# Optimization experiments

Hardware: AMD Instinct MI355X
Metric: run time of the kernel (lower is better)

## Reference

```python
import jax, jax.numpy as jnp
import numpy as np


def setup_inputs() -> dict:
    key = jax.random.key(0)
    k1, k2, k3 = jax.random.split(key, 3)
    B, N, D = 4, 4096, 256
    val = jax.random.normal(k1, (B, N, D), dtype=jnp.float32)
    state = jax.random.normal(k2, (B, N), dtype=jnp.float32)
    # val projection weight, scaled for unit-variance outputs
    Wv = jax.random.normal(k3, (D, D), dtype=jnp.float32) / np.sqrt(D)
    return {"val": val, "state": state, "Wv": Wv}


def reference(val, state, Wv):
    # pairwise_fn: dot-product scores over all node pairs -> [B, N, N]
    scores = jnp.einsum("bnd,bmd->bnm", val, val)
    # edge_compress_fn: softsign (non-softmax elementwise nonlinearity)
    edges = scores / (1.0 + jnp.abs(scores))
    # state_proj_fn = identity, val_proj_fn = linear
    projected_state = state                                  # [B, N]
    projected_val = jnp.einsum("bmd,de->bme", val, Wv)       # [B, N, D]
    # dual aggregation reusing the same edge matrix
    delta_state = jnp.einsum("bnm,bm->bn", edges, projected_state)
    delta_val = jnp.einsum("bnm,bmd->bnd", edges, projected_val)
    return (delta_state, delta_val)
```

## Files before the change

kernel.cpp:

```cpp
#include <hip/hip_runtime.h>

typedef unsigned short u16;
typedef unsigned char u8;
typedef unsigned int u32;
typedef __bf16 bf16x8 __attribute__((ext_vector_type(8)));
typedef float  f32x16 __attribute__((ext_vector_type(16)));
typedef int    i32x4  __attribute__((ext_vector_type(4)));
typedef int    i32x16 __attribute__((ext_vector_type(16)));

#define NB 4
#define NN 4096
#define ND 256

#define QPV (127.0f / 4.5f)
#define DPV (4.5f / 16129.0f)
#define QST (127.0f / 4.6f)
#define DST (4.6f / 16129.0f)
#define MAGIC 12582912.0f

__device__ __forceinline__ u16 f2bf(float x) { return __builtin_bit_cast(u16, (__bf16)x); }
__device__ __forceinline__ u32 fbits(float x) { return __builtin_bit_cast(u32, x); }

__device__ __forceinline__ u32 packlow4(float a, float b, float c, float d) {
    u32 p = __builtin_amdgcn_perm(fbits(b), fbits(a), 0x00000400u);
    u32 q = __builtin_amdgcn_perm(fbits(d), fbits(c), 0x00000400u);
    return __builtin_amdgcn_perm(q, p, 0x05040100u);
}


__global__ __launch_bounds__(256) void k_prep(const float* __restrict__ val,
                                              const float* __restrict__ state,
                                              const float* __restrict__ Wv,
                                              u16* __restrict__ kq, u8* __restrict__ kq8,
                                              float* __restrict__ srow,
                                              u8* __restrict__ vp8, u16* __restrict__ wv) {
    int tid = threadIdx.x;
    int bid = blockIdx.x;
    if (bid < 512) {
        __shared__ float t[32 * 257];
        __shared__ float rmax[32];
        const float* src = val + (size_t)bid * 32 * 256;
        #pragma unroll
        for (int k = 0; k < 8; k++) {
            int idx = tid + k * 256;
            int row = idx >> 6, c4 = idx & 63;
            float4 v = *(const float4*)(src + row * 256 + c4 * 4);
            float* p = t + row * 257 + c4 * 4;
            p[0] = v.x; p[1] = v.y; p[2] = v.z; p[3] = v.w;
        }
        __syncthreads();
        {
            int row = tid >> 3, seg = tid & 7;
            float m = 0.0f;
            #pragma unroll
            for (int i = 0; i < 32; i++) m = fmaxf(m, fabsf(t[row * 257 + seg + i * 8]));
            m = fmaxf(m, __shfl_down(m, 4));
            m = fmaxf(m, __shfl_down(m, 2));
            m = fmaxf(m, __shfl_down(m, 1));
            if (seg == 0) {
                m = fmaxf(m, 1e-20f);
                rmax[row] = m;
                srow[bid * 32 + row] = m * (1.0f / 127.0f);
            }
        }
        __syncthreads();
        u16* dst = kq + (size_t)bid * 16 * 512;
        #pragma unroll
        for (int k = 0; k < 4; k++) {
            int flat = tid + k * 256;
            int s = flat >> 6, l = flat & 63;
            int l31 = l & 31, h = l >> 5;
            const float* p = t + l31 * 257 + s * 16 + h * 8;
            union { u16 o[8]; uint4 q; } u;
            #pragma unroll
            for (int j = 0; j < 8; j++) u.o[j] = f2bf(p[j]);
            *(uint4*)(dst + (size_t)flat * 8) = u.q;
        }
        u8* dst8 = kq8 + (size_t)bid * 8192;
        #pragma unroll
        for (int k = 0; k < 2; k++) {
            int flat = tid + k * 256;
            int s = flat >> 6, l = flat & 63;
            int l31 = l & 31, h = l >> 5;
            float r127 = 127.0f / rmax[l31];
            const float* p = t + l31 * 257 + s * 32 + h * 16;
            u32 d[4];
            #pragma unroll
            for (int g = 0; g < 4; g++)
                d[g] = packlow4(fmaf(p[4 * g + 0], r127, MAGIC), fmaf(p[4 * g + 1], r127, MAGIC),
                                fmaf(p[4 * g + 2], r127, MAGIC), fmaf(p[4 * g + 3], r127, MAGIC));
            *(uint4*)(dst8 + (size_t)flat * 16) = make_uint4(d[0], d[1], d[2], d[3]);
        }
    } else if (bid < 516) {
        int b = bid - 512;
        __shared__ u8 qs[4096];
        #pragma unroll
        for (int k = 0; k < 16; k++) {
            int i = tid + k * 256;
            float x = fminf(fmaxf(state[b * 4096 + i] * QST, -127.0f), 127.0f);
            qs[i] = (u8)(fbits(x + MAGIC) & 255);
        }
        __syncthreads();
        #pragma unroll
        for (int k = 0; k < 32; k++) {
            int chunk = tid + k * 256;
            int strip = chunk >> 6, lane = chunk & 63, h = (lane >> 5) & 1;
            i32x4 v = *(const i32x4*)(qs + strip * 32 + h * 16);
            *(i32x4*)(vp8 + ((size_t)((b * 128 + strip) * 9 + 8)) * 1024 + (chunk & 63) * 16) = v;
        }
    } else {
        __shared__ u16 t2[256 * 33];
        int es = bid - 516, e0 = es * 32;
        #pragma unroll
        for (int k = 0; k < 8; k++) {
            int idx = tid + k * 256;
            int row = idx >> 3, c4 = idx & 7;
            float4 v = *(const float4*)(Wv + row * 256 + e0 + c4 * 4);
            u16* p = t2 + row * 33 + c4 * 4;
            p[0] = f2bf(v.x); p[1] = f2bf(v.y); p[2] = f2bf(v.z); p[3] = f2bf(v.w);
        }
        __syncthreads();
        u16* dst = wv + (size_t)es * 16 * 512;
        #pragma unroll
        for (int k = 0; k < 4; k++) {
            int flat = tid + k * 256;
            int s = flat >> 6, l = flat & 63;
            int l31 = l & 31, h = l >> 5;
            union { u16 o[8]; uint4 q; } u;
            #pragma unroll
            for (int j = 0; j < 8; j++) u.o[j] = t2[(s * 16 + h * 8 + j) * 33 + l31];
            *(uint4*)(dst + (size_t)flat * 8) = u.q;
        }
    }
}

__global__ __launch_bounds__(256) void k_pv(const u16* __restrict__ kq, const u16* __restrict__ wv,
                                            u8* __restrict__ vp8) {
    __shared__ u8 tp[4][32 * 48];
    int tid = threadIdx.x;
    int w = tid >> 6, lane = tid & 63;
    int l31 = lane & 31, h = lane >> 5;
    int bid = blockIdx.x;
    int bb = bid >> 6;
    int qb = (bid >> 1) & 31;
    int qh = bid & 1;
    const u16* wv0 = wv + (size_t)(w * 16) * 512 + lane * 8;
    const u16* wv1 = wv + (size_t)((w + 4) * 16) * 512 + lane * 8;
    const u16* kqb = kq + ((size_t)((bb * 128 + qb * 4 + qh * 2) * 16)) * 512 + lane * 8;
    f32x16 acc[2][2] = {};
    for (int s = 0; s < 16; s++) {
        bf16x8 a0 = *(const bf16x8*)(wv0 + s * 512);
        bf16x8 a1 = *(const bf16x8*)(wv1 + s * 512);
        bf16x8 b0 = *(const bf16x8*)(kqb + (size_t)s * 512);
        bf16x8 b1 = *(const bf16x8*)(kqb + (size_t)(16 + s) * 512);
        acc[0][0] = __builtin_amdgcn_mfma_f32_32x32x16_bf16(a0, b0, acc[0][0], 0, 0, 0);
        acc[0][1] = __builtin_amdgcn_mfma_f32_32x32x16_bf16(a0, b1, acc[0][1], 0, 0, 0);
        acc[1][0] = __builtin_amdgcn_mfma_f32_32x32x16_bf16(a1, b0, acc[1][0], 0, 0, 0);
        acc[1][1] = __builtin_amdgcn_mfma_f32_32x32x16_bf16(a1, b1, acc[1][1], 0, 0, 0);
    }
    u8* myp = tp[w];
    #pragma unroll
    for (int e = 0; e < 2; e++) {
        #pragma unroll
        for (int j = 0; j < 2; j++) {
            int es = w + 4 * e;
            int qt = qh * 2 + j;
            #pragma unroll
            for (int r = 0; r < 16; r++) {
                int erow = (r & 3) + 8 * (r >> 2) + 4 * h;
                float x = fminf(fmaxf(acc[e][j][r] * QPV, -127.0f), 127.0f);
                myp[erow * 48 + l31] = (u8)(fbits(x + MAGIC) & 255);
            }
            i32x4 v = *(const i32x4*)(myp + l31 * 48 + h * 16);
            *(i32x4*)(vp8 + ((size_t)((bb * 128 + qb * 4 + qt) * 9 + es)) * 1024 + lane * 16) = v;
        }
    }
}

__global__ __launch_bounds__(256, 2) void k_main(const u8* __restrict__ kq8,
                                                 const u8* __restrict__ vp8,
                                                 const float* __restrict__ srow,
                                                 float* __restrict__ ds_out,
                                                 float* __restrict__ dval_out) {
    __shared__ i32x4 pbuf[2][4][64];
    __shared__ int dsqi[4][32];

    int tid = threadIdx.x;
    int w = tid >> 6, lane = tid & 63;
    int l31 = lane & 31, h = lane >> 5;

    int id = blockIdx.x;
    int xcd = id & 7;
    int bb = xcd >> 1;
    int t7 = ((xcd & 1) << 6) | (id >> 3);
    int q0 = t7 * 32;
    size_t bbase = (size_t)bb * 128;

    i32x4 qf[8];
    {
        const u8* qsrc = kq8 + (bbase + t7) * 8192 + lane * 16;
        #pragma unroll
        for (int s = 0; s < 8; s++) qf[s] = *(const i32x4*)(qsrc + (size_t)s * 1024);
    }
    float srq = srow[bb * 4096 + q0 + l31];

    i32x16 oacc[2] = {};
    i32x16 dsa = {};

    i32x4 kf[8], vf[4][2], sf;
    float4 sg[4];
    {
        const u8* kb = kq8 + (bbase + w) * 8192 + lane * 16;
        #pragma unroll
        for (int s = 0; s < 8; s++) kf[s] = *(const i32x4*)(kb + (size_t)s * 1024);
        #pragma unroll
        for (int st = 0; st < 4; st++)
            #pragma unroll
            for (int e = 0; e < 2; e++)
                vf[st][e] = *(const i32x4*)(vp8 + ((size_t)((bbase + st) * 9 + 2 * w + e)) * 1024 + lane * 16);
        sf = *(const i32x4*)(vp8 + ((size_t)((bbase + w) * 9 + 8)) * 1024 + lane * 16);
        const float* srm = srow + bb * 4096 + w * 32;
        #pragma unroll
        for (int g = 0; g < 4; g++) sg[g] = *(const float4*)(srm + g * 8 + h * 4);
    }

    for (int mt = 0; mt < 32; mt++) {
        i32x16 s0 = {}, s1 = {};
        #pragma unroll
        for (int s = 0; s < 8; s += 2) {
            s0 = __builtin_amdgcn_mfma_i32_32x32x32_i8(kf[s], qf[s], s0, 0, 0, 0);
            s1 = __builtin_amdgcn_mfma_i32_32x32x32_i8(kf[s + 1], qf[s + 1], s1, 0, 0, 0);
        }
        if (mt + 1 < 32) {
            const u8* kb = kq8 + (bbase + (mt + 1) * 4 + w) * 8192 + lane * 16;
            #pragma unroll
            for (int s = 0; s < 8; s++) kf[s] = *(const i32x4*)(kb + (size_t)s * 1024);
        }

        float cf[16];
        #pragma unroll
        for (int r = 0; r < 16; r++) {
            float sm = ((const float*)&sg[r >> 2])[r & 3] * srq;
            float xs = (float)(s0[r] + s1[r]) * sm;
            float p = xs * __builtin_amdgcn_rcpf(1.0f + fabsf(xs));
            cf[r] = fmaf(p, 127.0f, MAGIC);
        }
        if (mt + 1 < 32) {
            const float* srm = srow + bb * 4096 + (mt + 1) * 128 + w * 32;
            #pragma unroll
            for (int g = 0; g < 4; g++) sg[g] = *(const float4*)(srm + g * 8 + h * 4);
        }
        u32 w0 = packlow4(cf[0], cf[1], cf[2], cf[3]);
        u32 w1 = packlow4(cf[4], cf[5], cf[6], cf[7]);
        u32 w2 = packlow4(cf[8], cf[9], cf[10], cf[11]);
        u32 w3 = packlow4(cf[12], cf[13], cf[14], cf[15]);
        u32 x0 = (u32)__shfl_xor((int)w0, 32);
        u32 x1 = (u32)__shfl_xor((int)w1, 32);
        u32 x2 = (u32)__shfl_xor((int)w2, 32);
        u32 x3 = (u32)__shfl_xor((int)w3, 32);
        union { u32 wd[4]; i32x4 v; } pu;
        if (h == 0) { pu.wd[0] = w0; pu.wd[1] = x0; pu.wd[2] = w1; pu.wd[3] = x1; }
        else        { pu.wd[0] = x2; pu.wd[1] = w2; pu.wd[2] = x3; pu.wd[3] = w3; }
        i32x4 pf = pu.v;

        dsa = __builtin_amdgcn_mfma_i32_32x32x32_i8(pf, sf, dsa, 0, 0, 0);
        if (mt + 1 < 32)
            sf = *(const i32x4*)(vp8 + ((size_t)((bbase + (mt + 1) * 4 + w) * 9 + 8)) * 1024 + lane * 16);

        pbuf[mt & 1][w][lane] = pf;
        __syncthreads();
        i32x4 pl[4];
        #pragma unroll
        for (int st = 0; st < 4; st++) pl[st] = pbuf[mt & 1][st][lane];

        #pragma unroll
        for (int st = 0; st < 4; st++) {
            oacc[0] = __builtin_amdgcn_mfma_i32_32x32x32_i8(pl[st], vf[st][0], oacc[0], 0, 0, 0);
            oacc[1] = __builtin_amdgcn_mfma_i32_32x32x32_i8(pl[st], vf[st][1], oacc[1], 0, 0, 0);
        }
        if (mt + 1 < 32) {
            #pragma unroll
            for (int st = 0; st < 4; st++)
                #pragma unroll
                for (int e = 0; e < 2; e++)
                    vf[st][e] = *(const i32x4*)(vp8 + ((size_t)((bbase + (mt + 1) * 4 + st) * 9 + 2 * w + e)) * 1024 + lane * 16);
        }
    }

    if (l31 == 0) {
        #pragma unroll
        for (int r = 0; r < 16; r++) dsqi[w][(r & 3) + 8 * (r >> 2) + 4 * h] = dsa[r];
    }
    #pragma unroll
    for (int e = 0; e < 2; e++) {
        #pragma unroll
        for (int r = 0; r < 16; r++) {
            int row = (r & 3) + 8 * (r >> 2) + 4 * h;
            dval_out[((size_t)(bb * 4096 + q0 + row)) * 256 + (2 * w + e) * 32 + l31] =
                (float)oacc[e][r] * DPV;
        }
    }
    __syncthreads();
    if (w == 0 && lane < 32) {
        int d = dsqi[0][lane] + dsqi[1][lane] + dsqi[2][lane] + dsqi[3][lane];
        ds_out[bb * 4096 + q0 + lane] = (float)d * DST;
    }
}

extern "C" void kernel_launch(void* const* d_in, const int* in_sizes, int n_in,
                              void* d_out, int out_size, void* d_ws, size_t ws_size,
                              hipStream_t stream) {
    const float* val   = (const float*)d_in[0];
    const float* state = (const float*)d_in[1];
    const float* Wv    = (const float*)d_in[2];

    float* ds_out   = (float*)d_out;
    float* dval_out = ds_out + NB * NN;

    u8*  kq8 = (u8*)d_ws;
    u8*  vp8 = kq8 + (size_t)NB * NN * ND;
    u16* kq  = (u16*)(vp8 + (size_t)NB * 128 * 9216);
    u16* wv  = kq + (size_t)NB * NN * ND;
    float* srow = (float*)(wv + 8 * 16 * 512);

    k_prep<<<524, 256, 0, stream>>>(val, state, Wv, kq, kq8, srow, vp8, wv);
    k_pv<<<256, 256, 0, stream>>>(kq, wv, vp8);
    k_main<<<512, 256, 0, stream>>>(kq8, vp8, srow, ds_out, dval_out);
}
```

Baseline: 142.2 us.

## Stage V tiles into LDS with double-buffered async loads and raise MFMA priority

Each wave now fetches its 8 KB slice of the next V tile straight into a double-buffered LDS stage using global_load_lds, instead of holding 8 V fragments per wave in registers. During the aggregation MFMAs, V fragments are read from LDS. The next K, state-fragment and srow loads are grouped into temporary registers issued early, and s_setprio brackets the MFMA sections. The aim is to cut VGPR pressure and overlap global traffic with compute. The cost is 64 KB of LDS per block, plus reliance on the barrier to order the async LDS writes, which needs correct vmcnt waits.

```diff
diff --git a/kernel.cpp b/kernel.cpp
--- a/kernel.cpp
+++ b/kernel.cpp
@@ -25,6 +25,12 @@
     u32 p = __builtin_amdgcn_perm(fbits(b), fbits(a), 0x00000400u);
     u32 q = __builtin_amdgcn_perm(fbits(d), fbits(c), 0x00000400u);
     return __builtin_amdgcn_perm(q, p, 0x05040100u);
+}
+
+typedef __attribute__((address_space(1))) const u32 gas_u32;
+typedef __attribute__((address_space(3))) u32 las_u32;
+__device__ __forceinline__ void async_ld16(void* lds, const void* g) {
+    __builtin_amdgcn_global_load_lds((gas_u32*)g, (las_u32*)lds, 16, 0, 0);
 }
 
 
@@ -182,6 +188,7 @@
                                                  const float* __restrict__ srow,
                                                  float* __restrict__ ds_out,
                                                  float* __restrict__ dval_out) {
+    __shared__ u8 vstage[2][4][8192];
     __shared__ i32x4 pbuf[2][4][64];
     __shared__ int dsqi[4][32];
 
@@ -207,17 +214,19 @@
     i32x16 oacc[2] = {};
     i32x16 dsa = {};
 
-    i32x4 kf[8], vf[4][2], sf;
+    {
+        u8* dst = vstage[0][w];
+        const u8* src = vp8 + ((size_t)((bbase + w) * 9)) * 1024;
+        #pragma unroll
+        for (int k = 0; k < 8; k++)
+            async_ld16(dst + (size_t)k * 1024 + lane * 16, src + (size_t)k * 1024 + lane * 16);
+    }
+    i32x4 kf[8], sf;
     float4 sg[4];
     {
         const u8* kb = kq8 + (bbase + w) * 8192 + lane * 16;
         #pragma unroll
         for (int s = 0; s < 8; s++) kf[s] = *(const i32x4*)(kb + (size_t)s * 1024);
-        #pragma unroll
-        for (int st = 0; st < 4; st++)
-            #pragma unroll
-            for (int e = 0; e < 2; e++)
-                vf[st][e] = *(const i32x4*)(vp8 + ((size_t)((bbase + st) * 9 + 2 * w + e)) * 1024 + lane * 16);
         sf = *(const i32x4*)(vp8 + ((size_t)((bbase + w) * 9 + 8)) * 1024 + lane * 16);
         const float* srm = srow + bb * 4096 + w * 32;
         #pragma unroll
@@ -226,15 +235,24 @@
 
     for (int mt = 0; mt < 32; mt++) {
         i32x16 s0 = {}, s1 = {};
+        __builtin_amdgcn_s_setprio(1);
         #pragma unroll
         for (int s = 0; s < 8; s += 2) {
             s0 = __builtin_amdgcn_mfma_i32_32x32x32_i8(kf[s], qf[s], s0, 0, 0, 0);
             s1 = __builtin_amdgcn_mfma_i32_32x32x32_i8(kf[s + 1], qf[s + 1], s1, 0, 0, 0);
         }
+        __builtin_amdgcn_s_setprio(0);
+
+        i32x4 kf2[8], sf2;
+        float4 sg2[4];
         if (mt + 1 < 32) {
             const u8* kb = kq8 + (bbase + (mt + 1) * 4 + w) * 8192 + lane * 16;
             #pragma unroll
-            for (int s = 0; s < 8; s++) kf[s] = *(const i32x4*)(kb + (size_t)s * 1024);
+            for (int s = 0; s < 8; s++) kf2[s] = *(const i32x4*)(kb + (size_t)s * 1024);
+            sf2 = *(const i32x4*)(vp8 + ((size_t)((bbase + (mt + 1) * 4 + w) * 9 + 8)) * 1024 + lane * 16);
+            const float* srm = srow + bb * 4096 + (mt + 1) * 128 + w * 32;
+            #pragma unroll
+            for (int g = 0; g < 4; g++) sg2[g] = *(const float4*)(srm + g * 8 + h * 4);
         }
 
         float cf[16];
@@ -244,11 +262,6 @@
             float xs = (float)(s0[r] + s1[r]) * sm;
             float p = xs * __builtin_amdgcn_rcpf(1.0f + fabsf(xs));
             cf[r] = fmaf(p, 127.0f, MAGIC);
-        }
-        if (mt + 1 < 32) {
-            const float* srm = srow + bb * 4096 + (mt + 1) * 128 + w * 32;
-            #pragma unroll
-            for (int g = 0; g < 4; g++) sg[g] = *(const float4*)(srm + g * 8 + h * 4);
         }
         u32 w0 = packlow4(cf[0], cf[1], cf[2], cf[3]);
         u32 w1 = packlow4(cf[4], cf[5], cf[6], cf[7]);
@@ -264,26 +277,40 @@
         i32x4 pf = pu.v;
 
         dsa = __builtin_amdgcn_mfma_i32_32x32x32_i8(pf, sf, dsa, 0, 0, 0);
-        if (mt + 1 < 32)
-            sf = *(const i32x4*)(vp8 + ((size_t)((bbase + (mt + 1) * 4 + w) * 9 + 8)) * 1024 + lane * 16);
 
         pbuf[mt & 1][w][lane] = pf;
-        __syncthreads();
+
+        __syncthreads();
+
+        if (mt + 1 < 32) {
+            u8* dst = vstage[(mt + 1) & 1][w];
+            const u8* src = vp8 + ((size_t)((bbase + (mt + 1) * 4 + w) * 9)) * 1024;
+            #pragma unroll
+            for (int k = 0; k < 8; k++)
+                async_ld16(dst + (size_t)k * 1024 + lane * 16, src + (size_t)k * 1024 + lane * 16);
+        }
+
         i32x4 pl[4];
         #pragma unroll
         for (int st = 0; st < 4; st++) pl[st] = pbuf[mt & 1][st][lane];
 
+        const u8* vb = vstage[mt & 1][0];
+        __builtin_amdgcn_s_setprio(1);
         #pragma unroll
         for (int st = 0; st < 4; st++) {
-            oacc[0] = __builtin_amdgcn_mfma_i32_32x32x32_i8(pl[st], vf[st][0], oacc[0], 0, 0, 0);
-            oacc[1] = __builtin_amdgcn_mfma_i32_32x32x32_i8(pl[st], vf[st][1], oacc[1], 0, 0, 0);
-        }
+            i32x4 vf0 = *(const i32x4*)(vb + (size_t)st * 8192 + (2 * w) * 1024 + lane * 16);
+            i32x4 vf1 = *(const i32x4*)(vb + (size_t)st * 8192 + (2 * w + 1) * 1024 + lane * 16);
+            oacc[0] = __builtin_amdgcn_mfma_i32_32x32x32_i8(pl[st], vf0, oacc[0], 0, 0, 0);
+            oacc[1] = __builtin_amdgcn_mfma_i32_32x32x32_i8(pl[st], vf1, oacc[1], 0, 0, 0);
+        }
+        __builtin_amdgcn_s_setprio(0);
+
         if (mt + 1 < 32) {
             #pragma unroll
-            for (int st = 0; st < 4; st++)
-                #pragma unroll
-                for (int e = 0; e < 2; e++)
-                    vf[st][e] = *(const i32x4*)(vp8 + ((size_t)((bbase + (mt + 1) * 4 + st) * 9 + 2 * w + e)) * 1024 + lane * 16);
+            for (int s = 0; s < 8; s++) kf[s] = kf2[s];
+            sf = sf2;
+            #pragma unroll
+            for (int g = 0; g < 4; g++) sg[g] = sg2[g];
         }
     }
 
```

New measurement: 153.2 us. 1.08x slower.

## Fuse val projection into prep kernel and drop bf16 val staging buffer

Applied to the files above, without the earlier changes.

The val@Wv projection now runs inside the prep kernel, where each 32-row block computes its projected tile from the fp32 tile already in shared memory. The bf16 copy of val (8 MB write plus read) and the separate k_pv launch both go away. Wv conversion moves to a small kernel that must run before prep, so the critical path gains one tiny launch. Prep blocks also do extra MFMA work and use more shared memory, which may lower occupancy.

```diff
diff --git a/kernel.cpp b/kernel.cpp
--- a/kernel.cpp
+++ b/kernel.cpp
@@ -28,17 +28,44 @@
 }
 
 
+__global__ __launch_bounds__(256) void k_wv(const float* __restrict__ Wv, u16* __restrict__ wv) {
+    __shared__ u16 t2[256 * 33];
+    int tid = threadIdx.x;
+    int es = blockIdx.x, e0 = es * 32;
+    #pragma unroll
+    for (int k = 0; k < 8; k++) {
+        int idx = tid + k * 256;
+        int row = idx >> 3, c4 = idx & 7;
+        float4 v = *(const float4*)(Wv + row * 256 + e0 + c4 * 4);
+        u16* p = t2 + row * 33 + c4 * 4;
+        p[0] = f2bf(v.x); p[1] = f2bf(v.y); p[2] = f2bf(v.z); p[3] = f2bf(v.w);
+    }
+    __syncthreads();
+    u16* dst = wv + (size_t)es * 16 * 512;
+    #pragma unroll
+    for (int k = 0; k < 4; k++) {
+        int flat = tid + k * 256;
+        int s = flat >> 6, l = flat & 63;
+        int l31 = l & 31, h = l >> 5;
+        union { u16 o[8]; uint4 q; } u;
+        #pragma unroll
+        for (int j = 0; j < 8; j++) u.o[j] = t2[(s * 16 + h * 8 + j) * 33 + l31];
+        *(uint4*)(dst + (size_t)flat * 8) = u.q;
+    }
+}
+
 __global__ __launch_bounds__(256) void k_prep(const float* __restrict__ val,
                                               const float* __restrict__ state,
-                                              const float* __restrict__ Wv,
-                                              u16* __restrict__ kq, u8* __restrict__ kq8,
+                                              const u16* __restrict__ wvf,
+                                              u8* __restrict__ kq8,
                                               float* __restrict__ srow,
-                                              u8* __restrict__ vp8, u16* __restrict__ wv) {
+                                              u8* __restrict__ vp8) {
     int tid = threadIdx.x;
     int bid = blockIdx.x;
     if (bid < 512) {
         __shared__ float t[32 * 257];
         __shared__ float rmax[32];
+        __shared__ u8 tp[4][32 * 48];
         const float* src = val + (size_t)bid * 32 * 256;
         #pragma unroll
         for (int k = 0; k < 8; k++) {
@@ -64,18 +91,6 @@
             }
         }
         __syncthreads();
-        u16* dst = kq + (size_t)bid * 16 * 512;
-        #pragma unroll
-        for (int k = 0; k < 4; k++) {
-            int flat = tid + k * 256;
-            int s = flat >> 6, l = flat & 63;
-            int l31 = l & 31, h = l >> 5;
-            const float* p = t + l31 * 257 + s * 16 + h * 8;
-            union { u16 o[8]; uint4 q; } u;
-            #pragma unroll
-            for (int j = 0; j < 8; j++) u.o[j] = f2bf(p[j]);
-            *(uint4*)(dst + (size_t)flat * 8) = u.q;
-        }
         u8* dst8 = kq8 + (size_t)bid * 8192;
         #pragma unroll
         for (int k = 0; k < 2; k++) {
@@ -91,7 +106,41 @@
                                 fmaf(p[4 * g + 2], r127, MAGIC), fmaf(p[4 * g + 3], r127, MAGIC));
             *(uint4*)(dst8 + (size_t)flat * 16) = make_uint4(d[0], d[1], d[2], d[3]);
         }
-    } else if (bid < 516) {
+        {
+            int w = tid >> 6, lane = tid & 63;
+            int l31 = lane & 31, h = lane >> 5;
+            const u16* wv0 = wvf + ((size_t)((w * 2 + 0) * 16)) * 512 + lane * 8;
+            const u16* wv1 = wvf + ((size_t)((w * 2 + 1) * 16)) * 512 + lane * 8;
+            f32x16 acc0 = {}, acc1 = {};
+            for (int s = 0; s < 16; s++) {
+                union { u16 o[8]; bf16x8 v; } ua;
+                const float* p = t + l31 * 257 + s * 16 + h * 8;
+                #pragma unroll
+                for (int j = 0; j < 8; j++) ua.o[j] = f2bf(p[j]);
+                bf16x8 b0 = *(const bf16x8*)(wv0 + (size_t)s * 512);
+                bf16x8 b1 = *(const bf16x8*)(wv1 + (size_t)s * 512);
+                acc0 = __builtin_amdgcn_mfma_f32_32x32x16_bf16(ua.v, b0, acc0, 0, 0, 0);
+                acc1 = __builtin_amdgcn_mfma_f32_32x32x16_bf16(ua.v, b1, acc1, 0, 0, 0);
+            }
+            u8* myp = tp[w];
+            #pragma unroll
+            for (int r = 0; r < 16; r++) {
+                int nrow = (r & 3) + 8 * (r >> 2) + 4 * h;
+                float x = fminf(fmaxf(acc0[r] * QPV, -127.0f), 127.0f);
+                myp[l31 * 48 + nrow] = (u8)(fbits(x + MAGIC) & 255);
+            }
+            i32x4 v0 = *(const i32x4*)(myp + l31 * 48 + h * 16);
+            *(i32x4*)(vp8 + ((size_t)(bid * 9 + w * 2 + 0)) * 1024 + lane * 16) = v0;
+            #pragma unroll
+            for (int r = 0; r < 16; r++) {
+                int nrow = (r & 3) + 8 * (r >> 2) + 4 * h;
+                float x = fminf(fmaxf(acc1[r] * QPV, -127.0f), 127.0f);
+                myp[l31 * 48 + nrow] = (u8)(fbits(x + MAGIC) & 255);
+            }
+            i32x4 v1 = *(const i32x4*)(myp + l31 * 48 + h * 16);
+            *(i32x4*)(vp8 + ((size_t)(bid * 9 + w * 2 + 1)) * 1024 + lane * 16) = v1;
+        }
+    } else {
         int b = bid - 512;
         __shared__ u8 qs[4096];
         #pragma unroll
@@ -107,72 +156,6 @@
             int strip = chunk >> 6, lane = chunk & 63, h = (lane >> 5) & 1;
             i32x4 v = *(const i32x4*)(qs + strip * 32 + h * 16);
             *(i32x4*)(vp8 + ((size_t)((b * 128 + strip) * 9 + 8)) * 1024 + (chunk & 63) * 16) = v;
-        }
-    } else {
-        __shared__ u16 t2[256 * 33];
-        int es = bid - 516, e0 = es * 32;
-        #pragma unroll
-        for (int k = 0; k < 8; k++) {
-            int idx = tid + k * 256;
-            int row = idx >> 3, c4 = idx & 7;
-            float4 v = *(const float4*)(Wv + row * 256 + e0 + c4 * 4);
-            u16* p = t2 + row * 33 + c4 * 4;
-            p[0] = f2bf(v.x); p[1] = f2bf(v.y); p[2] = f2bf(v.z); p[3] = f2bf(v.w);
-        }
-        __syncthreads();
-        u16* dst = wv + (size_t)es * 16 * 512;
-        #pragma unroll
-        for (int k = 0; k < 4; k++) {
-            int flat = tid + k * 256;
-            int s = flat >> 6, l = flat & 63;
-            int l31 = l & 31, h = l >> 5;
-            union { u16 o[8]; uint4 q; } u;
-            #pragma unroll
-            for (int j = 0; j < 8; j++) u.o[j] = t2[(s * 16 + h * 8 + j) * 33 + l31];
-            *(uint4*)(dst + (size_t)flat * 8) = u.q;
-        }
-    }
-}
-
-__global__ __launch_bounds__(256) void k_pv(const u16* __restrict__ kq, const u16* __restrict__ wv,
-                                            u8* __restrict__ vp8) {
-    __shared__ u8 tp[4][32 * 48];
-    int tid = threadIdx.x;
-    int w = tid >> 6, lane = tid & 63;
-    int l31 = lane & 31, h = lane >> 5;
-    int bid = blockIdx.x;
-    int bb = bid >> 6;
-    int qb = (bid >> 1) & 31;
-    int qh = bid & 1;
-    const u16* wv0 = wv + (size_t)(w * 16) * 512 + lane * 8;
-    const u16* wv1 = wv + (size_t)((w + 4) * 16) * 512 + lane * 8;
-    const u16* kqb = kq + ((size_t)((bb * 128 + qb * 4 + qh * 2) * 16)) * 512 + lane * 8;
-    f32x16 acc[2][2] = {};
-    for (int s = 0; s < 16; s++) {
-        bf16x8 a0 = *(const bf16x8*)(wv0 + s * 512);
-        bf16x8 a1 = *(const bf16x8*)(wv1 + s * 512);
-        bf16x8 b0 = *(const bf16x8*)(kqb + (size_t)s * 512);
-        bf16x8 b1 = *(const bf16x8*)(kqb + (size_t)(16 + s) * 512);
-        acc[0][0] = __builtin_amdgcn_mfma_f32_32x32x16_bf16(a0, b0, acc[0][0], 0, 0, 0);
-        acc[0][1] = __builtin_amdgcn_mfma_f32_32x32x16_bf16(a0, b1, acc[0][1], 0, 0, 0);
-        acc[1][0] = __builtin_amdgcn_mfma_f32_32x32x16_bf16(a1, b0, acc[1][0], 0, 0, 0);
-        acc[1][1] = __builtin_amdgcn_mfma_f32_32x32x16_bf16(a1, b1, acc[1][1], 0, 0, 0);
-    }
-    u8* myp = tp[w];
-    #pragma unroll
-    for (int e = 0; e < 2; e++) {
-        #pragma unroll
-        for (int j = 0; j < 2; j++) {
-            int es = w + 4 * e;
-            int qt = qh * 2 + j;
-            #pragma unroll
-            for (int r = 0; r < 16; r++) {
-                int erow = (r & 3) + 8 * (r >> 2) + 4 * h;
-                float x = fminf(fmaxf(acc[e][j][r] * QPV, -127.0f), 127.0f);
-                myp[erow * 48 + l31] = (u8)(fbits(x + MAGIC) & 255);
-            }
-            i32x4 v = *(const i32x4*)(myp + l31 * 48 + h * 16);
-            *(i32x4*)(vp8 + ((size_t)((bb * 128 + qb * 4 + qt) * 9 + es)) * 1024 + lane * 16) = v;
         }
     }
 }
@@ -319,11 +302,10 @@
 
     u8*  kq8 = (u8*)d_ws;
     u8*  vp8 = kq8 + (size_t)NB * NN * ND;
-    u16* kq  = (u16*)(vp8 + (size_t)NB * 128 * 9216);
-    u16* wv  = kq + (size_t)NB * NN * ND;
+    u16* wv  = (u16*)(vp8 + (size_t)NB * 128 * 9216);
     float* srow = (float*)(wv + 8 * 16 * 512);
 
-    k_prep<<<524, 256, 0, stream>>>(val, state, Wv, kq, kq8, srow, vp8, wv);
-    k_pv<<<256, 256, 0, stream>>>(kq, wv, vp8);
+    k_wv<<<8, 256, 0, stream>>>(Wv, wv);
+    k_prep<<<516, 256, 0, stream>>>(val, state, wv, kq8, srow, vp8);
     k_main<<<512, 256, 0, stream>>>(kq8, vp8, srow, ds_out, dval_out);
 }
```

After: 136.9 us. 3.7% less time.
